# Kernel tuning notes

Measured on AMD Instinct MI355X. Metric: run time of the kernel, lower is better.

## Reference

```python
import jax, jax.numpy as jnp
import numpy as np
import math

D_MODEL = 1024
N_HEADS = 16
D_HEAD = D_MODEL // N_HEADS
D_FF = 4 * D_MODEL
EPS = 1e-5


def layer_norm(x, gamma, beta):
    mu = jnp.mean(x, axis=-1, keepdims=True)
    var = jnp.var(x, axis=-1, keepdims=True)
    return (x - mu) * jax.lax.rsqrt(var + EPS) * gamma + beta


def setup_inputs() -> dict:
    key = jax.random.key(0)
    ks = jax.random.split(key, 8)
    B, C, D = 32, 256, D_MODEL
    s = 0.02
    return {
        "X": jax.random.normal(ks[0], (B, C, D), dtype=jnp.float32),
        "W_qkv": jax.random.normal(ks[1], (D, 3 * D), dtype=jnp.float32) * s,
        "b_qkv": jnp.zeros((3 * D,), dtype=jnp.float32),
        "W_proj": jax.random.normal(ks[2], (D, D), dtype=jnp.float32) * s,
        "b_proj": jnp.zeros((D,), dtype=jnp.float32),
        "g1": jnp.ones((D,), dtype=jnp.float32),
        "beta1": jnp.zeros((D,), dtype=jnp.float32),
        "g2": jnp.ones((D,), dtype=jnp.float32),
        "beta2": jnp.zeros((D,), dtype=jnp.float32),
        "W_ff1": jax.random.normal(ks[3], (D, D_FF), dtype=jnp.float32) * s,
        "b_ff1": jnp.zeros((D_FF,), dtype=jnp.float32),
        "W_ff2": jax.random.normal(ks[4], (D_FF, D), dtype=jnp.float32) * s,
        "b_ff2": jnp.zeros((D,), dtype=jnp.float32),
    }


def reference(X, W_qkv, b_qkv, W_proj, b_proj, g1, beta1, g2, beta2,
              W_ff1, b_ff1, W_ff2, b_ff2):
    B, C, D = X.shape
    H, Dh = N_HEADS, D_HEAD
    scale = 1.0 / math.sqrt(Dh)

    Xn = layer_norm(X, g1, beta1)
    qkv = Xn @ W_qkv + b_qkv                       # [B, C, 3D]
    q, k, v = jnp.split(qkv, 3, axis=-1)
    # split heads -> [B, H, C, Dh]
    sh = lambda t: t.reshape(B, C, H, Dh).transpose(0, 2, 1, 3)
    q, k, v = sh(q), sh(k), sh(v)

    scores = jnp.einsum("bhcd,bhkd->bhck", q, k) * scale  # [B, H, C, C]
    attn = jax.nn.softmax(scores, axis=-1)
    ctx = jnp.einsum("bhck,bhkd->bhcd", attn, v)           # [B, H, C, Dh]
    ctx = ctx.transpose(0, 2, 1, 3).reshape(B, C, D)

    X1 = X + (ctx @ W_proj + b_proj)
    X2n = layer_norm(X1, g2, beta2)
    h = jax.nn.gelu(X2n @ W_ff1 + b_ff1, approximate=False)
    X_out = X1 + (h @ W_ff2 + b_ff2)
    A = attn.mean(axis=1)                                   # [B, C, C]
    return (X_out, A)
```

## Files before the change

kernel.cpp:

```cpp
#include <hip/hip_runtime.h>
#include <cstdint>
#include <cstddef>

typedef short bf16x8 __attribute__((ext_vector_type(8)));
typedef float f32x4 __attribute__((ext_vector_type(4)));
typedef unsigned short u16;
typedef u16 u16x8 __attribute__((ext_vector_type(8)));

#define GLD16(gptr, lptr)                                                            \
  __builtin_amdgcn_global_load_lds((const __attribute__((address_space(1))) void*)(gptr), \
                                   (__attribute__((address_space(3))) void*)(lptr), 16, 0, 0)

__device__ __forceinline__ u16 f2bf(float f) {
  union { float f; unsigned u; } v; v.f = f;
  unsigned r = v.u + 0x7FFF + ((v.u >> 16) & 1);
  return (u16)(r >> 16);
}
__device__ __forceinline__ float bf2f(u16 h) {
  union { unsigned u; float f; } v; v.u = ((unsigned)h) << 16;
  return v.f;
}

template <int N> __device__ __forceinline__ void vmwait() {
  if constexpr (N == 0) asm volatile("s_waitcnt vmcnt(0)" ::: "memory");
  else if constexpr (N == 3) asm volatile("s_waitcnt vmcnt(3)" ::: "memory");
  else if constexpr (N == 4) asm volatile("s_waitcnt vmcnt(4)" ::: "memory");
  else if constexpr (N == 6) asm volatile("s_waitcnt vmcnt(6)" ::: "memory");
  else asm volatile("s_waitcnt vmcnt(8)" ::: "memory");
}

__device__ __forceinline__ bf16x8 lds_read_sw64(const u16* base, int row, int col) {
  int byt = row * 128 + col * 2;
  byt ^= (row & 7) << 4;
  return *(const bf16x8*)((const char*)base + byt);
}

__global__ __launch_bounds__(256) void transpose_cast(const float* __restrict__ in,
                                                      u16* __restrict__ out, int R, int C) {
  __shared__ float tile[32][33];
  const int tx = threadIdx.x, ty = threadIdx.y;
  const int c0 = blockIdx.x * 32, r0 = blockIdx.y * 32;
#pragma unroll
  for (int i = 0; i < 32; i += 8)
    tile[ty + i][tx] = in[(size_t)(r0 + ty + i) * C + c0 + tx];
  __syncthreads();
#pragma unroll
  for (int i = 0; i < 32; i += 8)
    out[(size_t)(c0 + ty + i) * R + r0 + tx] = f2bf(tile[tx][ty + i]);
}

__global__ __launch_bounds__(256) void layernorm_bf16(const float* __restrict__ X,
                                                      const float* __restrict__ g,
                                                      const float* __restrict__ be,
                                                      u16* __restrict__ out) {
  const int row = blockIdx.x, t = threadIdx.x;
  const int lane = t & 63, wave = t >> 6;
  const float* x = X + (size_t)row * 1024;
  __shared__ float part[4];
  float v[4]; float s = 0.f;
#pragma unroll
  for (int i = 0; i < 4; ++i) { v[i] = x[t + i * 256]; s += v[i]; }
#pragma unroll
  for (int o = 32; o >= 1; o >>= 1) s += __shfl_xor(s, o);
  if (lane == 0) part[wave] = s;
  __syncthreads();
  const float mu = (part[0] + part[1] + part[2] + part[3]) * (1.f / 1024.f);
  float d2 = 0.f;
#pragma unroll
  for (int i = 0; i < 4; ++i) { float d = v[i] - mu; d2 += d * d; }
#pragma unroll
  for (int o = 32; o >= 1; o >>= 1) d2 += __shfl_xor(d2, o);
  __syncthreads();
  if (lane == 0) part[wave] = d2;
  __syncthreads();
  const float var = (part[0] + part[1] + part[2] + part[3]) * (1.f / 1024.f);
  const float rstd = rsqrtf(var + 1e-5f);
#pragma unroll
  for (int i = 0; i < 4; ++i) {
    const int c = t + i * 256;
    out[(size_t)row * 1024 + c] = f2bf((v[i] - mu) * rstd * g[c] + be[c]);
  }
}

template <int EPI, int WM, int WN, int MF, int NF>
__global__ __launch_bounds__(512, 2) void gemm_pipe(const u16* __restrict__ A,
                                                    const u16* __restrict__ Bt,
                                                    const float* __restrict__ bias,
                                                    const float* __restrict__ res,
                                                    float* __restrict__ outf,
                                                    u16* __restrict__ outb,
                                                    int M, int N, int K) {
  constexpr int BM = WM * MF * 16, BN = WN * NF * 16;
  constexpr int LA = BM / 128, LB = BN / 128, L = LA + LB;
  constexpr int ASZ = BM * 32, BSZ = BN * 32;
  __shared__ u16 lds[4 * (ASZ + BSZ)];

  const int t = threadIdx.x, lane = t & 63, wave = t >> 6;
  const int wm = wave / WN, wn = wave % WN;
  const int l15 = lane & 15, l16 = lane >> 4;

  const int lb = (blockIdx.x & 7) * ((int)gridDim.x >> 3) + ((int)blockIdx.x >> 3);
  const int NBN = N / BN;
  const int bm = (lb / NBN) * BM, bn = (lb % NBN) * BN;

  const u16* asrcj[LA];
  const u16* bsrcj[LB];
#pragma unroll
  for (int j = 0; j < LA; ++j)
    asrcj[j] = A + (size_t)(bm + j * 128 + (t >> 2)) * K + (t & 3) * 8;
#pragma unroll
  for (int j = 0; j < LB; ++j)
    bsrcj[j] = Bt + (size_t)(bn + j * 128 + (t >> 2)) * K + (t & 3) * 8;

  auto stage = [&](int p) {
    const int koff = p * 32;
    char* abase = (char*)lds + (p & 3) * (ASZ * 2) + wave * 1024;
    char* bbase = (char*)lds + 8 * ASZ + (p & 3) * (BSZ * 2) + wave * 1024;
#pragma unroll
    for (int j = 0; j < LA; ++j) GLD16(asrcj[j] + koff, abase + j * 8192);
#pragma unroll
    for (int j = 0; j < LB; ++j) GLD16(bsrcj[j] + koff, bbase + j * 8192);
  };

  int aoff[MF], boff[NF];
#pragma unroll
  for (int m = 0; m < MF; ++m) aoff[m] = (wm * MF * 16 + m * 16 + l15) * 32 + l16 * 8;
#pragma unroll
  for (int n = 0; n < NF; ++n) boff[n] = (wn * NF * 16 + n * 16 + l15) * 32 + l16 * 8;

  const int nkt = K >> 5;
#pragma unroll
  for (int p = 0; p < 3; ++p) stage(p);

  f32x4 acc[MF][NF] = {};

#pragma unroll 1
  for (int kt = 0; kt < nkt; ++kt) {
    const int rem = nkt - 1 - kt;
    if (rem >= 2) vmwait<2 * L>();
    else if (rem == 1) vmwait<L>();
    else vmwait<0>();
    __builtin_amdgcn_s_barrier();
    __builtin_amdgcn_sched_barrier(0);
    if (rem >= 3) stage(kt + 3);

    const u16* ab = lds + (kt & 3) * ASZ;
    const u16* bb = lds + 4 * ASZ + (kt & 3) * BSZ;
    bf16x8 a[MF], b[NF];
#pragma unroll
    for (int m = 0; m < MF; ++m) a[m] = *(const bf16x8*)(ab + aoff[m]);
#pragma unroll
    for (int n = 0; n < NF; ++n) b[n] = *(const bf16x8*)(bb + boff[n]);
    __builtin_amdgcn_s_setprio(1);
#pragma unroll
    for (int m = 0; m < MF; ++m)
#pragma unroll
      for (int n = 0; n < NF; ++n)
        acc[m][n] = __builtin_amdgcn_mfma_f32_16x16x32_bf16(a[m], b[n], acc[m][n], 0, 0, 0);
    __builtin_amdgcn_s_setprio(0);
  }

  const int r0 = l16 * 4;
#pragma unroll
  for (int m = 0; m < MF; ++m) {
#pragma unroll
    for (int n = 0; n < NF; ++n) {
      const int col = bn + wn * NF * 16 + n * 16 + l15;
      const float bv = bias[col];
#pragma unroll
      for (int r = 0; r < 4; ++r) {
        const int row = bm + wm * MF * 16 + m * 16 + r0 + r;
        const float v = acc[m][n][r] + bv;
        const size_t o = (size_t)row * N + col;
        if (EPI == 0) {
          outb[o] = f2bf(v);
        } else if (EPI == 1) {
          outf[o] = res[o] + v;
        } else {
          const float u = 0.7978845608f * (v + 0.044715f * v * v * v);
          const float e = __expf(2.f * u);
          const float th = 1.f - 2.f / (1.f + e);
          outb[o] = f2bf(0.5f * v * (1.f + th));
        }
      }
    }
  }
}

__global__ __launch_bounds__(256) void attn_scores(const u16* __restrict__ qkv,
                                                   u16* __restrict__ probs) {
  __shared__ u16 Ks[256 * 64];
  __shared__ u16 Qs[64 * 64];
  const int t = threadIdx.x, lane = t & 63, wave = t >> 6;
  const int qb = blockIdx.x * 64, h = blockIdx.y, b = blockIdx.z;
  const size_t row0 = (size_t)b * 256 * 3072;

#pragma unroll
  for (int is = 0; is < 8; ++is) {
    int L = (is * 2048 + t * 8) * 2;
    int x = (L ^ ((L >> 3) & 0x70)) >> 1;
    int kk = x >> 6, d = x & 63;
    const u16* gp = qkv + row0 + (size_t)kk * 3072 + 1024 + h * 64 + d;
    GLD16(gp, (char*)Ks + is * 4096 + wave * 1024);
  }
#pragma unroll
  for (int is = 0; is < 2; ++is) {
    int L = (is * 2048 + t * 8) * 2;
    int x = (L ^ ((L >> 3) & 0x70)) >> 1;
    int q = x >> 6, d = x & 63;
    const u16* gp = qkv + row0 + (size_t)(qb + q) * 3072 + h * 64 + d;
    GLD16(gp, (char*)Qs + is * 4096 + wave * 1024);
  }
  __syncthreads();

  f32x4 acc[16] = {};
  bf16x8 aq[2];
#pragma unroll
  for (int ks = 0; ks < 2; ++ks)
    aq[ks] = lds_read_sw64(Qs, wave * 16 + (lane & 15), ks * 32 + (lane >> 4) * 8);
#pragma unroll
  for (int nf = 0; nf < 16; ++nf) {
#pragma unroll
    for (int ks = 0; ks < 2; ++ks) {
      bf16x8 bk = lds_read_sw64(Ks, nf * 16 + (lane & 15), ks * 32 + (lane >> 4) * 8);
      acc[nf] = __builtin_amdgcn_mfma_f32_16x16x32_bf16(aq[ks], bk, acc[nf], 0, 0, 0);
    }
  }

  const int r0 = (lane >> 4) * 4, cc = lane & 15;
  const float sc = 0.125f;
#pragma unroll
  for (int r = 0; r < 4; ++r) {
    float mx = -1e30f;
#pragma unroll
    for (int nf = 0; nf < 16; ++nf) mx = fmaxf(mx, acc[nf][r]);
#pragma unroll
    for (int o = 8; o >= 1; o >>= 1) mx = fmaxf(mx, __shfl_xor(mx, o));
    float s = 0.f;
#pragma unroll
    for (int nf = 0; nf < 16; ++nf) {
      float e = __expf((acc[nf][r] - mx) * sc);
      acc[nf][r] = e; s += e;
    }
#pragma unroll
    for (int o = 8; o >= 1; o >>= 1) s += __shfl_xor(s, o);
    const float rinv = 1.f / s;
    const int qrow = qb + wave * 16 + r0 + r;
    u16* prow = probs + (size_t)((b * 16 + h) * 256 + qrow) * 256;
#pragma unroll
    for (int nf = 0; nf < 16; ++nf)
      prow[nf * 16 + cc] = f2bf(acc[nf][r] * rinv);
  }
}

__global__ __launch_bounds__(256) void amean(const u16* __restrict__ probs,
                                             float* __restrict__ A) {
  const int bq = blockIdx.x;
  const int b = bq >> 8, q = bq & 255;
  const int t = threadIdx.x;
  float s = 0.f;
#pragma unroll
  for (int h = 0; h < 16; ++h)
    s += bf2f(probs[(size_t)((b * 16 + h) * 256 + q) * 256 + t]);
  A[(size_t)bq * 256 + t] = s * (1.f / 16.f);
}

__global__ __launch_bounds__(256) void attn_pv(const u16* __restrict__ qkv,
                                               const u16* __restrict__ probs,
                                               u16* __restrict__ ctx) {
  __shared__ u16 Vs[64 * 256];
  const int t = threadIdx.x, lane = t & 63, wave = t >> 6;
  const int h = blockIdx.x, b = blockIdx.y;

#pragma unroll
  for (int p = 0; p < 8; ++p) {
    int idx = p * 2048 + t * 8;
    int kk = idx >> 6, d0 = idx & 63;
    u16x8 vv = *(const u16x8*)(qkv + (size_t)(b * 256 + kk) * 3072 + 2048 + h * 64 + d0);
#pragma unroll
    for (int j = 0; j < 8; ++j) {
      int d = d0 + j;
      int byt = (d * 512 + kk * 2) ^ ((d & 7) << 4);
      *(u16*)((char*)Vs + byt) = vv[j];
    }
  }
  __syncthreads();

  f32x4 acc[4][4] = {};
  const u16* Pb = probs + (size_t)((b * 16 + h) * 256) * 256;
  const int cc = lane & 15, kg = (lane >> 4) * 8;
#pragma unroll
  for (int kt = 0; kt < 8; ++kt) {
    bf16x8 a[4], v[4];
#pragma unroll
    for (int m = 0; m < 4; ++m)
      a[m] = *(const bf16x8*)(Pb + (size_t)(wave * 64 + m * 16 + cc) * 256 + kt * 32 + kg);
#pragma unroll
    for (int n = 0; n < 4; ++n) {
      int d = n * 16 + cc;
      int kk = kt * 32 + kg;
      int byt = (d * 512 + kk * 2) ^ ((d & 7) << 4);
      v[n] = *(const bf16x8*)((const char*)Vs + byt);
    }
#pragma unroll
    for (int m = 0; m < 4; ++m)
#pragma unroll
      for (int n = 0; n < 4; ++n)
        acc[m][n] = __builtin_amdgcn_mfma_f32_16x16x32_bf16(a[m], v[n], acc[m][n], 0, 0, 0);
  }

  const int r0 = (lane >> 4) * 4;
#pragma unroll
  for (int m = 0; m < 4; ++m) {
    const int q = wave * 64 + m * 16 + r0;
#pragma unroll
    for (int n = 0; n < 4; ++n) {
      const int col = h * 64 + n * 16 + cc;
#pragma unroll
      for (int r = 0; r < 4; ++r)
        ctx[(size_t)(b * 256 + q + r) * 1024 + col] = f2bf(acc[m][n][r]);
    }
  }
}

extern "C" void kernel_launch(void* const* d_in, const int* in_sizes, int n_in,
                              void* d_out, int out_size, void* d_ws, size_t ws_size,
                              hipStream_t stream) {
  const float* X      = (const float*)d_in[0];
  const float* W_qkv  = (const float*)d_in[1];
  const float* b_qkv  = (const float*)d_in[2];
  const float* W_proj = (const float*)d_in[3];
  const float* b_proj = (const float*)d_in[4];
  const float* g1     = (const float*)d_in[5];
  const float* beta1  = (const float*)d_in[6];
  const float* g2     = (const float*)d_in[7];
  const float* beta2  = (const float*)d_in[8];
  const float* W_ff1  = (const float*)d_in[9];
  const float* b_ff1  = (const float*)d_in[10];
  const float* W_ff2  = (const float*)d_in[11];
  const float* b_ff2  = (const float*)d_in[12];

  float* Xout = (float*)d_out;
  float* Aout = (float*)d_out + 8388608;

  char* ws = (char*)d_ws;
  const size_t MB = 1u << 20;
  u16* xn    = (u16*)(ws + 0);
  u16* wqkv  = (u16*)(ws + 16 * MB);
  u16* wproj = (u16*)(ws + 22 * MB);
  u16* wff1  = (u16*)(ws + 24 * MB);
  u16* wff2  = (u16*)(ws + 32 * MB);
  u16* qkv   = (u16*)(ws + 40 * MB);
  u16* probs = (u16*)(ws + 88 * MB);
  u16* hbuf  = probs;
  float* x1  = (float*)(ws + 152 * MB);
  u16* ctx   = xn;
  u16* x1n   = xn;

  const dim3 tb(32, 8);
  transpose_cast<<<dim3(96, 32),  tb, 0, stream>>>(W_qkv,  wqkv, 1024, 3072);
  transpose_cast<<<dim3(32, 32),  tb, 0, stream>>>(W_proj, wproj, 1024, 1024);
  transpose_cast<<<dim3(128, 32), tb, 0, stream>>>(W_ff1,  wff1, 1024, 4096);
  transpose_cast<<<dim3(32, 128), tb, 0, stream>>>(W_ff2,  wff2, 4096, 1024);

  layernorm_bf16<<<8192, 256, 0, stream>>>(X, g1, beta1, xn);

  gemm_pipe<0, 4, 2, 4, 4><<<768, 512, 0, stream>>>(xn, wqkv, b_qkv, nullptr, nullptr, qkv,
                                                    8192, 3072, 1024);

  attn_scores<<<dim3(4, 16, 32), 256, 0, stream>>>(qkv, probs);
  amean<<<8192, 256, 0, stream>>>(probs, Aout);
  attn_pv<<<dim3(16, 32), 256, 0, stream>>>(qkv, probs, ctx);

  gemm_pipe<1, 4, 2, 4, 4><<<256, 512, 0, stream>>>(ctx, wproj, b_proj, X, x1, nullptr,
                                                    8192, 1024, 1024);

  layernorm_bf16<<<8192, 256, 0, stream>>>(x1, g2, beta2, x1n);

  gemm_pipe<2, 2, 4, 8, 4><<<512, 512, 0, stream>>>(x1n, wff1, b_ff1, nullptr, nullptr, hbuf,
                                                    8192, 4096, 1024);

  gemm_pipe<1, 4, 2, 4, 4><<<256, 512, 0, stream>>>(hbuf, wff2, b_ff2, x1, Xout, nullptr,
                                                    8192, 1024, 4096);
}
```

Measured before the change: 380.3 us.

## Rewrite GEMM mainloop to fixed 256x128 tile, BK=64, XOR-swizzled double-buffered LDS

Replaces the templated GEMM with a single 256x128 tile configuration. Each K step now covers 64 elements instead of 32, and an XOR-swizzled LDS layout is applied on the global-to-LDS load and mirrored on the reads to avoid bank conflicts. The pipeline drops from four buffers to two: each step loads all fragments, waits on lgkmcnt, takes an extra barrier, then prefetches the next stage before the MFMAs. This halves the number of loop iterations and barrier rounds per K and lowers bank conflicts. The cost is shallower prefetch depth and an extra barrier per iteration. The FF1 grid changes to 1024 blocks to match the smaller tile.

```diff
diff --git a/kernel.cpp b/kernel.cpp
--- a/kernel.cpp
+++ b/kernel.cpp
@@ -23,8 +23,6 @@
 
 template <int N> __device__ __forceinline__ void vmwait() {
   if constexpr (N == 0) asm volatile("s_waitcnt vmcnt(0)" ::: "memory");
-  else if constexpr (N == 3) asm volatile("s_waitcnt vmcnt(3)" ::: "memory");
-  else if constexpr (N == 4) asm volatile("s_waitcnt vmcnt(4)" ::: "memory");
   else if constexpr (N == 6) asm volatile("s_waitcnt vmcnt(6)" ::: "memory");
   else asm volatile("s_waitcnt vmcnt(8)" ::: "memory");
 }
@@ -82,7 +80,7 @@
   }
 }
 
-template <int EPI, int WM, int WN, int MF, int NF>
+template <int EPI>
 __global__ __launch_bounds__(512, 2) void gemm_pipe(const u16* __restrict__ A,
                                                     const u16* __restrict__ Bt,
                                                     const float* __restrict__ bias,
@@ -90,73 +88,86 @@
                                                     float* __restrict__ outf,
                                                     u16* __restrict__ outb,
                                                     int M, int N, int K) {
-  constexpr int BM = WM * MF * 16, BN = WN * NF * 16;
-  constexpr int LA = BM / 128, LB = BN / 128, L = LA + LB;
-  constexpr int ASZ = BM * 32, BSZ = BN * 32;
-  __shared__ u16 lds[4 * (ASZ + BSZ)];
+  constexpr int MF = 8, NF = 2;
+  constexpr int AT = 256 * 64, BT = 128 * 64;
+  __shared__ u16 lds[2 * (AT + BT)];
 
   const int t = threadIdx.x, lane = t & 63, wave = t >> 6;
-  const int wm = wave / WN, wn = wave % WN;
+  const int wm = wave >> 2, wn = wave & 3;
   const int l15 = lane & 15, l16 = lane >> 4;
 
   const int lb = (blockIdx.x & 7) * ((int)gridDim.x >> 3) + ((int)blockIdx.x >> 3);
-  const int NBN = N / BN;
-  const int bm = (lb / NBN) * BM, bn = (lb % NBN) * BN;
-
-  const u16* asrcj[LA];
-  const u16* bsrcj[LB];
-#pragma unroll
-  for (int j = 0; j < LA; ++j)
-    asrcj[j] = A + (size_t)(bm + j * 128 + (t >> 2)) * K + (t & 3) * 8;
-#pragma unroll
-  for (int j = 0; j < LB; ++j)
-    bsrcj[j] = Bt + (size_t)(bn + j * 128 + (t >> 2)) * K + (t & 3) * 8;
+  const int NBN = N >> 7;
+  const int bm = (lb / NBN) * 256, bn = (lb % NBN) * 128;
+
+  const u16* aptr[4];
+  const u16* bptr[2];
+#pragma unroll
+  for (int is = 0; is < 4; ++is) {
+    int Lb = is * 8192 + t * 16;
+    int x = (Lb ^ ((Lb >> 3) & 0x70)) >> 1;
+    aptr[is] = A + (size_t)(bm + (x >> 6)) * K + (x & 63);
+  }
+#pragma unroll
+  for (int is = 0; is < 2; ++is) {
+    int Lb = is * 8192 + t * 16;
+    int x = (Lb ^ ((Lb >> 3) & 0x70)) >> 1;
+    bptr[is] = Bt + (size_t)(bn + (x >> 6)) * K + (x & 63);
+  }
 
   auto stage = [&](int p) {
-    const int koff = p * 32;
-    char* abase = (char*)lds + (p & 3) * (ASZ * 2) + wave * 1024;
-    char* bbase = (char*)lds + 8 * ASZ + (p & 3) * (BSZ * 2) + wave * 1024;
-#pragma unroll
-    for (int j = 0; j < LA; ++j) GLD16(asrcj[j] + koff, abase + j * 8192);
-#pragma unroll
-    for (int j = 0; j < LB; ++j) GLD16(bsrcj[j] + koff, bbase + j * 8192);
+    const int ko = p * 64;
+    char* ab = (char*)lds + (p & 1) * (AT * 2) + t * 16;
+    char* bb = (char*)lds + 4 * AT + (p & 1) * (BT * 2) + t * 16;
+#pragma unroll
+    for (int is = 0; is < 4; ++is) GLD16(aptr[is] + ko, ab + is * 8192);
+#pragma unroll
+    for (int is = 0; is < 2; ++is) GLD16(bptr[is] + ko, bb + is * 8192);
   };
-
-  int aoff[MF], boff[NF];
-#pragma unroll
-  for (int m = 0; m < MF; ++m) aoff[m] = (wm * MF * 16 + m * 16 + l15) * 32 + l16 * 8;
-#pragma unroll
-  for (int n = 0; n < NF; ++n) boff[n] = (wn * NF * 16 + n * 16 + l15) * 32 + l16 * 8;
-
-  const int nkt = K >> 5;
-#pragma unroll
-  for (int p = 0; p < 3; ++p) stage(p);
+  stage(0); stage(1);
+
+  const int rx = (l15 & 7) << 4;
+  const int co0 = (l16 * 16) ^ rx;
+  const int co1 = (64 + l16 * 16) ^ rx;
 
   f32x4 acc[MF][NF] = {};
+  const int nkt = K >> 6;
 
 #pragma unroll 1
   for (int kt = 0; kt < nkt; ++kt) {
-    const int rem = nkt - 1 - kt;
-    if (rem >= 2) vmwait<2 * L>();
-    else if (rem == 1) vmwait<L>();
-    else vmwait<0>();
+    if (kt < nkt - 1) vmwait<6>(); else vmwait<0>();
     __builtin_amdgcn_s_barrier();
+
+    const char* Ab = (const char*)lds + (kt & 1) * (AT * 2);
+    const char* Bb = (const char*)lds + 4 * AT + (kt & 1) * (BT * 2);
+    bf16x8 af[MF][2], bfr[NF][2];
+#pragma unroll
+    for (int n = 0; n < NF; ++n) {
+      const int rb = (wn * NF * 16 + n * 16 + l15) * 128;
+      bfr[n][0] = *(const bf16x8*)(Bb + rb + co0);
+      bfr[n][1] = *(const bf16x8*)(Bb + rb + co1);
+    }
+#pragma unroll
+    for (int m = 0; m < MF; ++m) {
+      const int ra = (wm * MF * 16 + m * 16 + l15) * 128;
+      af[m][0] = *(const bf16x8*)(Ab + ra + co0);
+      af[m][1] = *(const bf16x8*)(Ab + ra + co1);
+    }
+    asm volatile("s_waitcnt lgkmcnt(0)" ::: "memory");
     __builtin_amdgcn_sched_barrier(0);
-    if (rem >= 3) stage(kt + 3);
-
-    const u16* ab = lds + (kt & 3) * ASZ;
-    const u16* bb = lds + 4 * ASZ + (kt & 3) * BSZ;
-    bf16x8 a[MF], b[NF];
-#pragma unroll
-    for (int m = 0; m < MF; ++m) a[m] = *(const bf16x8*)(ab + aoff[m]);
-#pragma unroll
-    for (int n = 0; n < NF; ++n) b[n] = *(const bf16x8*)(bb + boff[n]);
+    __builtin_amdgcn_s_barrier();
+
+    if (kt + 2 < nkt) stage(kt + 2);
+    __builtin_amdgcn_sched_barrier(0);
+
     __builtin_amdgcn_s_setprio(1);
 #pragma unroll
     for (int m = 0; m < MF; ++m)
 #pragma unroll
-      for (int n = 0; n < NF; ++n)
-        acc[m][n] = __builtin_amdgcn_mfma_f32_16x16x32_bf16(a[m], b[n], acc[m][n], 0, 0, 0);
+      for (int n = 0; n < NF; ++n) {
+        acc[m][n] = __builtin_amdgcn_mfma_f32_16x16x32_bf16(af[m][0], bfr[n][0], acc[m][n], 0, 0, 0);
+        acc[m][n] = __builtin_amdgcn_mfma_f32_16x16x32_bf16(af[m][1], bfr[n][1], acc[m][n], 0, 0, 0);
+      }
     __builtin_amdgcn_s_setprio(0);
   }
 
@@ -165,11 +176,11 @@
   for (int m = 0; m < MF; ++m) {
 #pragma unroll
     for (int n = 0; n < NF; ++n) {
-      const int col = bn + wn * NF * 16 + n * 16 + l15;
+      const int col = bn + wn * 32 + n * 16 + l15;
       const float bv = bias[col];
 #pragma unroll
       for (int r = 0; r < 4; ++r) {
-        const int row = bm + wm * MF * 16 + m * 16 + r0 + r;
+        const int row = bm + wm * 128 + m * 16 + r0 + r;
         const float v = acc[m][n][r] + bv;
         const size_t o = (size_t)row * N + col;
         if (EPI == 0) {
@@ -365,21 +376,21 @@
 
   layernorm_bf16<<<8192, 256, 0, stream>>>(X, g1, beta1, xn);
 
-  gemm_pipe<0, 4, 2, 4, 4><<<768, 512, 0, stream>>>(xn, wqkv, b_qkv, nullptr, nullptr, qkv,
-                                                    8192, 3072, 1024);
+  gemm_pipe<0><<<768, 512, 0, stream>>>(xn, wqkv, b_qkv, nullptr, nullptr, qkv,
+                                        8192, 3072, 1024);
 
   attn_scores<<<dim3(4, 16, 32), 256, 0, stream>>>(qkv, probs);
   amean<<<8192, 256, 0, stream>>>(probs, Aout);
   attn_pv<<<dim3(16, 32), 256, 0, stream>>>(qkv, probs, ctx);
 
-  gemm_pipe<1, 4, 2, 4, 4><<<256, 512, 0, stream>>>(ctx, wproj, b_proj, X, x1, nullptr,
-                                                    8192, 1024, 1024);
+  gemm_pipe<1><<<256, 512, 0, stream>>>(ctx, wproj, b_proj, X, x1, nullptr,
+                                        8192, 1024, 1024);
 
   layernorm_bf16<<<8192, 256, 0, stream>>>(x1, g2, beta2, x1n);
 
-  gemm_pipe<2, 2, 4, 8, 4><<<512, 512, 0, stream>>>(x1n, wff1, b_ff1, nullptr, nullptr, hbuf,
-                                                    8192, 4096, 1024);
-
-  gemm_pipe<1, 4, 2, 4, 4><<<256, 512, 0, stream>>>(hbuf, wff2, b_ff2, x1, Xout, nullptr,
-                                                    8192, 1024, 4096);
-}
+  gemm_pipe<2><<<1024, 512, 0, stream>>>(x1n, wff1, b_ff1, nullptr, nullptr, hbuf,
+                                         8192, 4096, 1024);
+
+  gemm_pipe<1><<<256, 512, 0, stream>>>(hbuf, wff2, b_ff2, x1, Xout, nullptr,
+                                        8192, 1024, 4096);
+}
```

Result: no change. 380.9 us (+0.2%).
